# Optimization experiments

Measured on AMD Instinct MI355X. Metric: run time of the kernel, lower is better.

## Reference

```python
import jax, jax.numpy as jnp
import numpy as np

KERNEL = 7
PAD = 3


def setup_inputs() -> dict:
    key = jax.random.key(0)
    k1, k2 = jax.random.split(key)
    x = jax.random.normal(k1, (32, 256, 112, 112), dtype=jnp.float32)
    # Conv2d(2, 1, 7, bias=False) weight, OIHW
    W = jax.random.normal(k2, (1, 2, KERNEL, KERNEL), dtype=jnp.float32) * 0.1
    return {"x": x, "W": W}


def reference(x, W):
    # channel-wise mean and max -> [B, 2, H, W]
    avg_out = jnp.mean(x, axis=1, keepdims=True)
    max_out = jnp.max(x, axis=1, keepdims=True)
    pooled = jnp.concatenate([avg_out, max_out], axis=1)
    # 2->1 conv, padding 3 (SAME for k=7)
    y = jax.lax.conv_general_dilated(
        pooled, W,
        window_strides=(1, 1),
        padding=[(PAD, PAD), (PAD, PAD)],
        dimension_numbers=("NCHW", "OIHW", "NCHW"),
    )
    return jax.nn.sigmoid(y)
```

## Files before the change

kernel.cpp:

```cpp
#include <hip/hip_runtime.h>
#include <math.h>

#define BATCH 32
#define CH    256
#define HH    112
#define WW    112
#define HW    (HH * WW)
#define HW4   (HW / 4)

#define CHUNK 448

typedef float f32x4 __attribute__((ext_vector_type(4)));

__global__ __launch_bounds__(448) void sa_pool_kernel(
    const f32x4* __restrict__ x4,
    f32x4* __restrict__ avg4,
    f32x4* __restrict__ max4)
{
    int tid = threadIdx.x;
    int b   = blockIdx.y;
    int q   = blockIdx.x * CHUNK + tid;

    const f32x4* p = x4 + (size_t)b * (CH * HW4) + q;

    int c0 = (blockIdx.x * 37 + blockIdx.y * 11) & (CH - 1);

    f32x4 s = (f32x4){0.f, 0.f, 0.f, 0.f};
    f32x4 m = (f32x4){-INFINITY, -INFINITY, -INFINITY, -INFINITY};

    #pragma unroll 8
    for (int cc = 0; cc < CH; ++cc) {
        int c = cc + c0;
        c -= (c >= CH) ? CH : 0;
        f32x4 v = __builtin_nontemporal_load(p + (size_t)c * HW4);
        s.x += v.x; s.y += v.y; s.z += v.z; s.w += v.w;
        m.x = fmaxf(m.x, v.x);
        m.y = fmaxf(m.y, v.y);
        m.z = fmaxf(m.z, v.z);
        m.w = fmaxf(m.w, v.w);
    }

    const float inv = 1.0f / (float)CH;
    f32x4 a;
    a.x = s.x * inv; a.y = s.y * inv; a.z = s.z * inv; a.w = s.w * inv;

    int g = b * HW4 + q;
    avg4[g] = a;
    max4[g] = m;
}

#define TILE 16
#define TW   (TILE + 6)

__global__ __launch_bounds__(256) void sa_conv_kernel(
    const float* __restrict__ avgp,
    const float* __restrict__ maxp,
    const float* __restrict__ wt,
    float* __restrict__ out)
{
    __shared__ float t0[TW][TW];
    __shared__ float t1[TW][TW];
    __shared__ float w[2][49];

    int tid = threadIdx.x;
    int b   = blockIdx.z;
    int ty0 = blockIdx.y * TILE;
    int tx0 = blockIdx.x * TILE;

    if (tid < 98) w[tid / 49][tid % 49] = wt[tid];

    const float* ap = avgp + b * HW;
    const float* mp = maxp + b * HW;

    for (int idx = tid; idx < TW * TW; idx += 256) {
        int iy = idx / TW;
        int ix = idx - iy * TW;
        int gy = ty0 + iy - 3;
        int gx = tx0 + ix - 3;
        bool ok = (gy >= 0) && (gy < HH) && (gx >= 0) && (gx < WW);
        int gofs = gy * WW + gx;
        t0[iy][ix] = ok ? ap[gofs] : 0.0f;
        t1[iy][ix] = ok ? mp[gofs] : 0.0f;
    }
    __syncthreads();

    int oy = tid >> 4;
    int ox = tid & 15;

    float acc = 0.0f;
    #pragma unroll
    for (int i = 0; i < 7; ++i) {
        #pragma unroll
        for (int j = 0; j < 7; ++j) {
            acc += w[0][i * 7 + j] * t0[oy + i][ox + j];
            acc += w[1][i * 7 + j] * t1[oy + i][ox + j];
        }
    }

    float y = 1.0f / (1.0f + expf(-acc));
    out[b * HW + (ty0 + oy) * WW + (tx0 + ox)] = y;
}

extern "C" void kernel_launch(void* const* d_in, const int* in_sizes, int n_in,
                              void* d_out, int out_size, void* d_ws, size_t ws_size,
                              hipStream_t stream)
{
    const float* x  = (const float*)d_in[0];
    const float* wt = (const float*)d_in[1];
    float* out = (float*)d_out;

    float* avgp = (float*)d_ws;
    float* maxp = avgp + (size_t)BATCH * HW;

    dim3 grid1(HW4 / CHUNK, BATCH);
    sa_pool_kernel<<<grid1, CHUNK, 0, stream>>>(
        (const f32x4*)x, (f32x4*)avgp, (f32x4*)maxp);

    dim3 grid2(WW / TILE, HH / TILE, BATCH);
    sa_conv_kernel<<<grid2, 256, 0, stream>>>(avgp, maxp, wt, out);
}
```

Baseline: 76.72 us.

## Fuse channel pooling and 7x7 conv into one cooperative kernel with grid sync

Merges the pooling and convolution kernels into a single cooperative launch of 224 blocks. After pooling, a grid-wide sync separates the phases, and each block then convolves a 16-row full-width strip, with each thread producing four outputs and a vector store. This removes the second kernel launch and its tail. In exchange, the pooling phase runs only 224 blocks of 448 threads, which may underuse the memory bandwidth of a 256-CU device, and grid sync adds its own cost.

```diff
diff --git a/kernel.cpp b/kernel.cpp
--- a/kernel.cpp
+++ b/kernel.cpp
@@ -1,5 +1,8 @@
 #include <hip/hip_runtime.h>
+#include <hip/hip_cooperative_groups.h>
 #include <math.h>
+
+namespace cg = cooperative_groups;
 
 #define BATCH 32
 #define CH    256
@@ -8,22 +11,31 @@
 #define HW    (HH * WW)
 #define HW4   (HW / 4)
 
+#define NBX   7
 #define CHUNK 448
+#define ROWS  16
 
 typedef float f32x4 __attribute__((ext_vector_type(4)));
 
-__global__ __launch_bounds__(448) void sa_pool_kernel(
+__global__ __launch_bounds__(448) void sa_fused_kernel(
     const f32x4* __restrict__ x4,
     f32x4* __restrict__ avg4,
-    f32x4* __restrict__ max4)
+    f32x4* __restrict__ max4,
+    const float* __restrict__ wt,
+    float* __restrict__ out)
 {
+    __shared__ float t0[22][120];
+    __shared__ float t1[22][120];
+    __shared__ float w[2][49];
+
     int tid = threadIdx.x;
-    int b   = blockIdx.y;
-    int q   = blockIdx.x * CHUNK + tid;
+    int blk = blockIdx.x;
+    int b   = blk / NBX;
+    int bx  = blk - b * NBX;
+    int q   = bx * CHUNK + tid;
 
     const f32x4* p = x4 + (size_t)b * (CH * HW4) + q;
-
-    int c0 = (blockIdx.x * 37 + blockIdx.y * 11) & (CH - 1);
+    int c0 = (bx * 37 + b * 11) & (CH - 1);
 
     f32x4 s = (f32x4){0.f, 0.f, 0.f, 0.f};
     f32x4 m = (f32x4){-INFINITY, -INFINITY, -INFINITY, -INFINITY};
@@ -47,36 +59,21 @@
     int g = b * HW4 + q;
     avg4[g] = a;
     max4[g] = m;
-}
 
-#define TILE 16
-#define TW   (TILE + 6)
-
-__global__ __launch_bounds__(256) void sa_conv_kernel(
-    const float* __restrict__ avgp,
-    const float* __restrict__ maxp,
-    const float* __restrict__ wt,
-    float* __restrict__ out)
-{
-    __shared__ float t0[TW][TW];
-    __shared__ float t1[TW][TW];
-    __shared__ float w[2][49];
-
-    int tid = threadIdx.x;
-    int b   = blockIdx.z;
-    int ty0 = blockIdx.y * TILE;
-    int tx0 = blockIdx.x * TILE;
+    __threadfence();
+    cg::this_grid().sync();
 
     if (tid < 98) w[tid / 49][tid % 49] = wt[tid];
 
-    const float* ap = avgp + b * HW;
-    const float* mp = maxp + b * HW;
+    const float* ap = (const float*)avg4 + (size_t)b * HW;
+    const float* mp = (const float*)max4 + (size_t)b * HW;
+    int r0 = bx * ROWS;
 
-    for (int idx = tid; idx < TW * TW; idx += 256) {
-        int iy = idx / TW;
-        int ix = idx - iy * TW;
-        int gy = ty0 + iy - 3;
-        int gx = tx0 + ix - 3;
+    for (int idx = tid; idx < 22 * 118; idx += 448) {
+        int iy = idx / 118;
+        int ix = idx - iy * 118;
+        int gy = r0 + iy - 3;
+        int gx = ix - 3;
         bool ok = (gy >= 0) && (gy < HH) && (gx >= 0) && (gx < WW);
         int gofs = gy * WW + gx;
         t0[iy][ix] = ok ? ap[gofs] : 0.0f;
@@ -84,38 +81,48 @@
     }
     __syncthreads();
 
-    int oy = tid >> 4;
-    int ox = tid & 15;
+    int row = (tid * 4) / WW;
+    int col = (tid * 4) % WW;
 
-    float acc = 0.0f;
+    float acc0 = 0.f, acc1 = 0.f, acc2 = 0.f, acc3 = 0.f;
     #pragma unroll
     for (int i = 0; i < 7; ++i) {
         #pragma unroll
-        for (int j = 0; j < 7; ++j) {
-            acc += w[0][i * 7 + j] * t0[oy + i][ox + j];
-            acc += w[1][i * 7 + j] * t1[oy + i][ox + j];
+        for (int k = 0; k < 7; ++k) {
+            float w0 = w[0][i * 7 + k];
+            float w1 = w[1][i * 7 + k];
+            const float* r0p = &t0[row + i][col + k];
+            const float* r1p = &t1[row + i][col + k];
+            acc0 += w0 * r0p[0] + w1 * r1p[0];
+            acc1 += w0 * r0p[1] + w1 * r1p[1];
+            acc2 += w0 * r0p[2] + w1 * r1p[2];
+            acc3 += w0 * r0p[3] + w1 * r1p[3];
         }
     }
 
-    float y = 1.0f / (1.0f + expf(-acc));
-    out[b * HW + (ty0 + oy) * WW + (tx0 + ox)] = y;
+    f32x4 o;
+    o.x = 1.0f / (1.0f + expf(-acc0));
+    o.y = 1.0f / (1.0f + expf(-acc1));
+    o.z = 1.0f / (1.0f + expf(-acc2));
+    o.w = 1.0f / (1.0f + expf(-acc3));
+    *((f32x4*)(out + (size_t)b * HW + (size_t)(r0 + row) * WW + col)) = o;
 }
 
 extern "C" void kernel_launch(void* const* d_in, const int* in_sizes, int n_in,
                               void* d_out, int out_size, void* d_ws, size_t ws_size,
                               hipStream_t stream)
 {
-    const float* x  = (const float*)d_in[0];
-    const float* wt = (const float*)d_in[1];
-    float* out = (float*)d_out;
+    const f32x4* x4   = (const f32x4*)d_in[0];
+    const float* wt   = (const float*)d_in[1];
+    float*       out  = (float*)d_out;
 
-    float* avgp = (float*)d_ws;
-    float* maxp = avgp + (size_t)BATCH * HW;
+    f32x4* avg4 = (f32x4*)d_ws;
+    f32x4* max4 = avg4 + (size_t)BATCH * HW4;
 
-    dim3 grid1(HW4 / CHUNK, BATCH);
-    sa_pool_kernel<<<grid1, CHUNK, 0, stream>>>(
-        (const f32x4*)x, (f32x4*)avgp, (f32x4*)maxp);
+    void* args[5] = { (void*)&x4, (void*)&avg4, (void*)&max4,
+                      (void*)&wt, (void*)&out };
 
-    dim3 grid2(WW / TILE, HH / TILE, BATCH);
-    sa_conv_kernel<<<grid2, 256, 0, stream>>>(avgp, maxp, wt, out);
+    hipLaunchCooperativeKernel((const void*)sa_fused_kernel,
+                               dim3(BATCH * NBX), dim3(CHUNK),
+                               args, 0, stream);
 }
```

New measurement: 158.7 us. 2.07x slower.
